# Performance work log

Measured on AMD Instinct MI355X. Metric: run time of the kernel, lower is better.

The kernel has to match this reference:

```python
import jax, jax.numpy as jnp
import numpy as np

TEMPERATURE = 0.1
EPS = 1e-8  # torch cosine_similarity eps
NEG_FILL = -9e15

def setup_inputs() -> dict:
    key = jax.random.key(0)
    stacked_batch = jax.random.normal(key, (8192, 128), dtype=jnp.float32)
    return {"stacked_batch": stacked_batch}

def reference(stacked_batch) -> jnp.ndarray:
    n = stacked_batch.shape[0]
    # cosine similarity = normalized GEMM (equivalent to torch broadcast form)
    norm = jnp.maximum(jnp.linalg.norm(stacked_batch, axis=-1, keepdims=True), EPS)
    z = stacked_batch / norm                      # [N, D]
    sim = jnp.matmul(z, z.T) / TEMPERATURE        # [N, N]
    # mask self-similarity on the diagonal
    idx = jnp.arange(n)
    sim = sim.at[idx, idx].set(NEG_FILL)
    # positive pair for row i is column (i + N/2) mod N
    pos_cols = (idx + n // 2) % n
    pos = sim[idx, pos_cols]                      # [N]
    loss = jax.scipy.special.logsumexp(sim, axis=-1) - pos
    return loss.mean()
```

## Files before the change

kernel.cpp:

```cpp
#include <hip/hip_runtime.h>
#include <hip/hip_bf16.h>

#define N 8192
#define D 128
#define HALF_N 4096
#define SQRT_SCALE_LOG2E 3.79828236f
#define LN2 0.693147180559945f

#define COLS_PER_ITER 64
#define ITERS 2
#define LDS_STRIDE 136

typedef short frag8 __attribute__((ext_vector_type(8)));
typedef float f32x4 __attribute__((ext_vector_type(4)));

#define OFF_POS 0
#define OFF_SUM N
#define OFF_ACC (2 * N)
#define OFF_CNT (2 * N + 1)
#define OFF_Z_BYTES ((2 * N + 64) * 4)

__device__ __forceinline__ unsigned short f2bf(float f) {
    unsigned int u = __float_as_uint(f);
    u += 0x7FFFu + ((u >> 16) & 1u);
    return (unsigned short)(u >> 16);
}

__global__ __launch_bounds__(256) void k_normalize(const float* __restrict__ x,
                                                   unsigned short* __restrict__ z,
                                                   float* __restrict__ wsf) {
    const int row  = blockIdx.x * 4 + (threadIdx.x >> 6);
    const int lane = threadIdx.x & 63;
    float2 v = ((const float2*)x)[row * 64 + lane];
    float s = v.x * v.x + v.y * v.y;
    #pragma unroll
    for (int m = 32; m >= 1; m >>= 1) s += __shfl_xor(s, m);
    float inv = SQRT_SCALE_LOG2E / fmaxf(sqrtf(s), 1e-8f);
    ushort2 o;
    o.x = f2bf(v.x * inv);
    o.y = f2bf(v.y * inv);
    ((ushort2*)z)[row * 64 + lane] = o;
    const int gid = blockIdx.x * 256 + threadIdx.x;
    if (gid < N + 2) wsf[OFF_SUM + gid] = 0.0f;
}

__global__ __launch_bounds__(256, 2) void k_simloss(const unsigned short* __restrict__ z,
                                                    float* __restrict__ sumexp,
                                                    float* __restrict__ pos) {
    __shared__ unsigned short lds[COLS_PER_ITER * LDS_STRIDE];

    const int tid  = threadIdx.x;
    const int wave = tid >> 6;
    const int lane = tid & 63;
    const int l15  = lane & 15;
    const int quad = lane >> 4;

    int b = blockIdx.x, bi = 0;
    while (b >= 64 - 2 * bi) { b -= 64 - 2 * bi; ++bi; }
    const int jh = 2 * bi + b;
    const int wrow = bi * 256 + wave * 64;
    const int colbase0 = jh * 128;

    frag8 a[4][4];
    #pragma unroll
    for (int s = 0; s < 4; ++s) {
        const uint4* p = (const uint4*)&z[(wrow + s * 16 + l15) * D + quad * 8];
        #pragma unroll
        for (int q = 0; q < 4; ++q) {
            uint4 t = p[q * 4];
            a[s][q] = *(frag8*)&t;
        }
    }

    float sums[4][4];
    #pragma unroll
    for (int s = 0; s < 4; ++s)
        #pragma unroll
        for (int r = 0; r < 4; ++r) sums[s][r] = 0.0f;

    for (int it = 0; it < ITERS; ++it) {
        const int colbase = colbase0 + it * COLS_PER_ITER;
        __syncthreads();
        #pragma unroll
        for (int u = 0; u < 4; ++u) {
            int idx = u * 256 + tid;
            int r   = idx >> 4;
            int c8  = idx & 15;
            uint4 t = *(const uint4*)&z[(colbase + r) * D + c8 * 8];
            *(uint4*)&lds[r * LDS_STRIDE + c8 * 8] = t;
        }
        __syncthreads();

        const bool active = (colbase >= wrow);
        const bool isSelf = (colbase == wrow);
        const bool isPos  = (colbase == wrow + HALF_N);
        if (!active) continue;

        const unsigned short* lp = &lds[l15 * LDS_STRIDE + quad * 8];

        #pragma unroll
        for (int c = 0; c < 4; ++c) {
            f32x4 acc[4];
            #pragma unroll
            for (int s = 0; s < 4; ++s) acc[s] = (f32x4){0.f, 0.f, 0.f, 0.f};
            #pragma unroll
            for (int q = 0; q < 4; ++q) {
                frag8 bf = *(const frag8*)(lp + c * 16 * LDS_STRIDE + q * 32);
                #pragma unroll
                for (int s = 0; s < 4; ++s)
                    acc[s] = __builtin_amdgcn_mfma_f32_16x16x32_bf16(a[s][q], bf, acc[s], 0, 0, 0);
            }
            float cs = 0.0f;
            if (isSelf | isPos) {
                #pragma unroll
                for (int s = 0; s < 4; ++s)
                    #pragma unroll
                    for (int r = 0; r < 4; ++r) {
                        float v = acc[s][r];
                        float e = __builtin_amdgcn_exp2f(v);
                        if (c == s) {
                            bool hit = (l15 == quad * 4 + r);
                            if (isSelf && hit) e = 0.0f;
                            if (isPos  && hit) pos[wrow + s * 16 + quad * 4 + r] = v * LN2;
                        }
                        sums[s][r] += e;
                        cs += e;
                    }
            } else {
                #pragma unroll
                for (int s = 0; s < 4; ++s)
                    #pragma unroll
                    for (int r = 0; r < 4; ++r) {
                        float e = __builtin_amdgcn_exp2f(acc[s][r]);
                        sums[s][r] += e;
                        cs += e;
                    }
            }
            if (!isSelf) {
                cs += __shfl_xor(cs, 16);
                cs += __shfl_xor(cs, 32);
                if (quad == 0)
                    atomicAdd(&sumexp[colbase + c * 16 + l15], cs);
            }
        }
    }

    #pragma unroll
    for (int s = 0; s < 4; ++s)
        #pragma unroll
        for (int r = 0; r < 4; ++r) {
            float v = sums[s][r];
            v += __shfl_xor(v, 1);
            v += __shfl_xor(v, 2);
            v += __shfl_xor(v, 4);
            v += __shfl_xor(v, 8);
            if (l15 == 0)
                atomicAdd(&sumexp[wrow + s * 16 + quad * 4 + r], v);
        }
}

__global__ __launch_bounds__(256) void k_rowloss(const float* __restrict__ sumexp,
                                                 const float* __restrict__ pos,
                                                 float* __restrict__ acc0,
                                                 unsigned int* __restrict__ counter,
                                                 float* __restrict__ out) {
    const int row = blockIdx.x * 256 + threadIdx.x;
    float loss = __logf(sumexp[row]) - pos[row & (HALF_N - 1)];
    #pragma unroll
    for (int m = 32; m >= 1; m >>= 1) loss += __shfl_xor(loss, m);
    __shared__ float p[4];
    if ((threadIdx.x & 63) == 0) p[threadIdx.x >> 6] = loss;
    __syncthreads();
    if (threadIdx.x == 0) {
        atomicAdd(acc0, p[0] + p[1] + p[2] + p[3]);
        __threadfence();
        unsigned prev = atomicAdd(counter, 1u);
        if (prev == gridDim.x - 1) {
            float total = atomicAdd(acc0, 0.0f);
            out[0] = total * (1.0f / N);
        }
    }
}

extern "C" void kernel_launch(void* const* d_in, const int* in_sizes, int n_in,
                              void* d_out, int out_size, void* d_ws, size_t ws_size,
                              hipStream_t stream) {
    const float* x = (const float*)d_in[0];
    float* wsf    = (float*)d_ws;
    float* pos    = wsf + OFF_POS;
    float* sumexp = wsf + OFF_SUM;
    float* acc0   = wsf + OFF_ACC;
    unsigned int* counter = (unsigned int*)(wsf + OFF_CNT);
    unsigned short* z = (unsigned short*)((char*)d_ws + OFF_Z_BYTES);

    k_normalize<<<N / 4, 256, 0, stream>>>(x, z, wsf);
    k_simloss<<<1056, 256, 0, stream>>>(z, sumexp, pos);
    k_rowloss<<<N / 256, 256, 0, stream>>>(sumexp, pos, acc0, counter, (float*)d_out);
}
```

Before: 85.60 us.

## Replace global atomic row/column sums with per-block partial sums reduced in rowloss

Each simloss block now accumulates its column exp-sums in shared memory and writes row and column partials to a dedicated per-block slot instead of issuing global atomicAdds. The rowloss kernel gathers these partials per row across the triangular block layout before taking the log. This removes atomic contention and the need to zero the sum buffer, at the cost of extra global writes and a strided gather in the final kernel. The final kernel is also launched with smaller 64-thread blocks.

```diff
diff --git a/kernel.cpp b/kernel.cpp
--- a/kernel.cpp
+++ b/kernel.cpp
@@ -7,24 +7,27 @@
 #define SQRT_SCALE_LOG2E 3.79828236f
 #define LN2 0.693147180559945f
 
+#define NUNITS 1056
 #define COLS_PER_ITER 64
-#define ITERS 2
 #define LDS_STRIDE 136
+#define UNIT_STRIDE 384
 
 typedef short frag8 __attribute__((ext_vector_type(8)));
 typedef float f32x4 __attribute__((ext_vector_type(4)));
 
 #define OFF_POS 0
-#define OFF_SUM N
-#define OFF_ACC (2 * N)
-#define OFF_CNT (2 * N + 1)
-#define OFF_Z_BYTES ((2 * N + 64) * 4)
+#define OFF_ACC N
+#define OFF_CNT (N + 1)
+#define OFF_PS  (N + 64)
+#define OFF_Z_BYTES ((OFF_PS + NUNITS * UNIT_STRIDE) * 4)
 
 __device__ __forceinline__ unsigned short f2bf(float f) {
     unsigned int u = __float_as_uint(f);
     u += 0x7FFFu + ((u >> 16) & 1u);
     return (unsigned short)(u >> 16);
 }
+
+__device__ __forceinline__ int unit_base(int bi) { return bi * (65 - bi); }
 
 __global__ __launch_bounds__(256) void k_normalize(const float* __restrict__ x,
                                                    unsigned short* __restrict__ z,
@@ -41,13 +44,14 @@
     o.y = f2bf(v.y * inv);
     ((ushort2*)z)[row * 64 + lane] = o;
     const int gid = blockIdx.x * 256 + threadIdx.x;
-    if (gid < N + 2) wsf[OFF_SUM + gid] = 0.0f;
+    if (gid < 2) wsf[OFF_ACC + gid] = 0.0f;
 }
 
 __global__ __launch_bounds__(256, 2) void k_simloss(const unsigned short* __restrict__ z,
-                                                    float* __restrict__ sumexp,
+                                                    float* __restrict__ psums,
                                                     float* __restrict__ pos) {
     __shared__ unsigned short lds[COLS_PER_ITER * LDS_STRIDE];
+    __shared__ float colacc[4][128];
 
     const int tid  = threadIdx.x;
     const int wave = tid >> 6;
@@ -60,6 +64,10 @@
     const int jh = 2 * bi + b;
     const int wrow = bi * 256 + wave * 64;
     const int colbase0 = jh * 128;
+    float* myps = &psums[blockIdx.x * UNIT_STRIDE];
+
+    colacc[wave][lane] = 0.0f;
+    colacc[wave][64 + lane] = 0.0f;
 
     frag8 a[4][4];
     #pragma unroll
@@ -78,7 +86,8 @@
         #pragma unroll
         for (int r = 0; r < 4; ++r) sums[s][r] = 0.0f;
 
-    for (int it = 0; it < ITERS; ++it) {
+    #pragma unroll
+    for (int it = 0; it < 2; ++it) {
         const int colbase = colbase0 + it * COLS_PER_ITER;
         __syncthreads();
         #pragma unroll
@@ -91,10 +100,9 @@
         }
         __syncthreads();
 
-        const bool active = (colbase >= wrow);
         const bool isSelf = (colbase == wrow);
         const bool isPos  = (colbase == wrow + HALF_N);
-        if (!active) continue;
+        if (colbase < wrow) continue;
 
         const unsigned short* lp = &lds[l15 * LDS_STRIDE + quad * 8];
 
@@ -140,7 +148,7 @@
                 cs += __shfl_xor(cs, 16);
                 cs += __shfl_xor(cs, 32);
                 if (quad == 0)
-                    atomicAdd(&sumexp[colbase + c * 16 + l15], cs);
+                    colacc[wave][it * 64 + c * 16 + l15] += cs;
             }
         }
     }
@@ -155,24 +163,36 @@
             v += __shfl_xor(v, 4);
             v += __shfl_xor(v, 8);
             if (l15 == 0)
-                atomicAdd(&sumexp[wrow + s * 16 + quad * 4 + r], v);
-        }
-}
-
-__global__ __launch_bounds__(256) void k_rowloss(const float* __restrict__ sumexp,
-                                                 const float* __restrict__ pos,
-                                                 float* __restrict__ acc0,
-                                                 unsigned int* __restrict__ counter,
-                                                 float* __restrict__ out) {
-    const int row = blockIdx.x * 256 + threadIdx.x;
-    float loss = __logf(sumexp[row]) - pos[row & (HALF_N - 1)];
+                myps[wave * 64 + s * 16 + quad * 4 + r] = v;
+        }
+
+    __syncthreads();
+    if (tid < 128)
+        myps[256 + tid] = colacc[0][tid] + colacc[1][tid] + colacc[2][tid] + colacc[3][tid];
+}
+
+__global__ __launch_bounds__(64) void k_rowloss(const float* __restrict__ psums,
+                                                const float* __restrict__ pos,
+                                                float* __restrict__ acc0,
+                                                unsigned int* __restrict__ counter,
+                                                float* __restrict__ out) {
+    const int r = blockIdx.x * 64 + threadIdx.x;
+    const int bi = r >> 8;
+    const int ubase = unit_base(bi);
+    const int nrow = 64 - 2 * bi;
+    float sum = 0.0f;
+    for (int k = 0; k < nrow; ++k)
+        sum += psums[(ubase + k) * UNIT_STRIDE + (r & 255)];
+    const int jh = r >> 7;
+    const int ncol = (jh >> 1) + 1;
+    for (int b2 = 0; b2 < ncol; ++b2)
+        sum += psums[(unit_base(b2) + (jh - 2 * b2)) * UNIT_STRIDE + 256 + (r & 127)];
+
+    float loss = __logf(sum) - pos[r & (HALF_N - 1)];
     #pragma unroll
     for (int m = 32; m >= 1; m >>= 1) loss += __shfl_xor(loss, m);
-    __shared__ float p[4];
-    if ((threadIdx.x & 63) == 0) p[threadIdx.x >> 6] = loss;
-    __syncthreads();
     if (threadIdx.x == 0) {
-        atomicAdd(acc0, p[0] + p[1] + p[2] + p[3]);
+        atomicAdd(acc0, loss);
         __threadfence();
         unsigned prev = atomicAdd(counter, 1u);
         if (prev == gridDim.x - 1) {
@@ -188,12 +208,12 @@
     const float* x = (const float*)d_in[0];
     float* wsf    = (float*)d_ws;
     float* pos    = wsf + OFF_POS;
-    float* sumexp = wsf + OFF_SUM;
     float* acc0   = wsf + OFF_ACC;
     unsigned int* counter = (unsigned int*)(wsf + OFF_CNT);
+    float* psums  = wsf + OFF_PS;
     unsigned short* z = (unsigned short*)((char*)d_ws + OFF_Z_BYTES);
 
     k_normalize<<<N / 4, 256, 0, stream>>>(x, z, wsf);
-    k_simloss<<<1056, 256, 0, stream>>>(z, sumexp, pos);
-    k_rowloss<<<N / 256, 256, 0, stream>>>(sumexp, pos, acc0, counter, (float*)d_out);
-}
+    k_simloss<<<NUNITS, 256, 0, stream>>>(z, psums, pos);
+    k_rowloss<<<N / 64, 64, 0, stream>>>(psums, pos, acc0, counter, (float*)d_out);
+}
```

Result: slower. 98.93 us (+15.6%).
